# Performance work log

Measured on AMD Instinct MI355X. Metric: run time of the kernel, lower is better.

## Reference

```python
import jax, jax.numpy as jnp
import numpy as np

N_NODES = 16384
N_EDGES = 262144
M = 32          # eq_latent_multiplicity
HD = 16         # attention_head_dim
INV_SQRTD = 1.0 / np.sqrt(HD)
CLIP = 5.0      # attention_logit_clip
EPS = 1e-6
# irreps 0e + 1o: component slices of the channel_wise [.., m, 4] layout
EQ_SLICES = [(0, 1), (1, 4)]
TP_SLICES = [(0, 1), (1, 4), (4, 7), (7, 8)]  # 0e, 1o, 1o, 0e outputs of the uuu tensor product


def so3_layernorm(x, slices):
    # per-irrep RMS over (multiplicity, components), equivariant since it only rescales blocks
    outs = []
    for a, b in slices:
        blk = x[..., a:b]
        rms = jnp.sqrt(jnp.mean(blk * blk, axis=(-2, -1), keepdims=True) + EPS)
        outs.append(blk / rms)
    return jnp.concatenate(outs, axis=-1)


def setup_inputs() -> dict:
    key = jax.random.key(0)
    ks = jax.random.split(key, 12)
    E, N = N_EDGES, N_NODES
    inp = {
        "scalar_latent": jax.random.normal(ks[0], (E, 128), jnp.float32),
        "equiv_latent": jax.random.normal(ks[1], (E, M, 4), jnp.float32),
        "node_invariants": jax.random.normal(ks[2], (N, 64), jnp.float32),
        "edge_conditioning": jax.random.normal(ks[3], (E, 16), jnp.float32),
        "update_coeff": jnp.ones((1,), jnp.float32),
        "W_env": jax.random.normal(ks[4], (128, M * 2), jnp.float32) / np.sqrt(128),
        "b_env": jnp.zeros((M * 2,), jnp.float32),
        "Wq": jax.random.normal(ks[5], (64, M * HD), jnp.float32) / np.sqrt(64),
        "Wk": jax.random.normal(ks[6], (128, M * HD), jnp.float32) / np.sqrt(128),
        "W_mix": jax.random.normal(ks[7], (2 * M + 16, M * 4), jnp.float32) / np.sqrt(2 * M + 16),
        "b_mix": jnp.zeros((M * 4,), jnp.float32),
        "W_sc": jax.random.normal(ks[8], (2 * M + 16, 128), jnp.float32) / np.sqrt(2 * M + 16),
        "b_sc": jnp.zeros((128,), jnp.float32),
        "edge_center": jax.random.randint(ks[9], (E,), 0, N, jnp.int32),
        "active_edges": jnp.arange(E, dtype=jnp.int32),
    }
    return inp


def _forward(scalar_latent, equiv_latent, node_invariants, edge_conditioning,
             update_coeff, W_env, b_env, Wq, Wk, W_mix, b_mix, W_sc, b_sc,
             edge_center, active_edges):
    E = scalar_latent.shape[0]
    N = node_invariants.shape[0]

    # env_embed_mlp: scalar-latent derived gates modulate each irrep block (EquivariantScalarMLP)
    g = jax.nn.silu(scalar_latent @ W_env + b_env).reshape(E, M, 2)
    env_edges = jnp.concatenate([
        equiv_latent[..., 0:1] * g[..., 0:1],   # 0e block
        equiv_latent[..., 1:4] * g[..., 1:2],   # 1o block
    ], axis=-1)  # [E, M, 4]

    # attention: Q from receiver-node invariants, K from per-edge scalar latent
    Q = (node_invariants[edge_center] @ Wq).reshape(E, M, HD)
    K = (scalar_latent @ Wk).reshape(E, M, HD)
    logits = jnp.einsum('emd,emd->em', Q, K) * INV_SQRTD
    logits = jnp.clip(logits, -CLIP, CLIP)
    # scatter_softmax over edges sharing the same center node, per head m
    mx = jax.ops.segment_max(logits, edge_center, num_segments=N)   # [N, M]
    z = jnp.exp(logits - mx[edge_center])
    denom = jax.ops.segment_sum(z, edge_center, num_segments=N)[edge_center]
    attn = z / denom                                               # [E, M]
    env_edges = env_edges * attn[..., None]

    # scatter_sum edges -> nodes, SO3 layer norm, gather back per edge
    env_nodes = jax.ops.segment_sum(env_edges, edge_center, num_segments=N)  # [N, M, 4]
    env_nodes = so3_layernorm(env_nodes, EQ_SLICES)
    local_env = env_nodes[edge_center]                                       # [E, M, 4]

    # Contracter uuu, no weights, component normalization; irreps 0e+1o x 0e+1o -> 0e,1o,1o,0e
    x0, x1 = equiv_latent[..., 0:1], equiv_latent[..., 1:4]
    y0, y1 = local_env[..., 0:1], local_env[..., 1:4]
    tp_out = jnp.concatenate([
        x0 * y0,                                                    # 0e
        x0 * y1,                                                    # 1o
        x1 * y0,                                                    # 1o
        jnp.sum(x1 * y1, axis=-1, keepdims=True) / np.sqrt(3.0),    # 0e
    ], axis=-1)  # [E, M, 8]
    tp_out = so3_layernorm(tp_out, TP_SLICES)

    # projection EquivariantScalarMLP with edge conditioning
    inv_feats = jnp.concatenate([tp_out[..., 0], tp_out[..., 7]], axis=-1)  # [E, 2M]
    feats = jnp.concatenate([inv_feats, edge_conditioning], axis=-1)        # [E, 2M+16]
    mix = (feats @ W_mix + b_mix).reshape(E, M, 4)
    new_equiv = jnp.concatenate([
        mix[..., 0:1] * tp_out[..., 0:1] + mix[..., 1:2] * tp_out[..., 7:8],
        mix[..., 2:3] * tp_out[..., 1:4] + mix[..., 3:4] * tp_out[..., 4:7],
    ], axis=-1)  # [E, M, 4]
    new_scalar = feats @ W_sc + b_sc  # [E, 128]

    # residual stream: apply_residual_stream
    c_old = jax.lax.rsqrt(update_coeff * update_coeff + 1.0)  # [1]
    c_new = update_coeff * c_old
    scalar_out = (c_old * scalar_latent).at[active_edges].add(c_new * new_scalar)
    equiv_out = (c_old[..., None] * equiv_latent).at[active_edges].add(c_new[..., None] * new_equiv)
    return scalar_out, equiv_out


def reference(scalar_latent, equiv_latent, node_invariants, edge_conditioning,
              update_coeff, W_env, b_env, Wq, Wk, W_mix, b_mix, W_sc, b_sc,
              edge_center, active_edges):
    return _forward(scalar_latent, equiv_latent, node_invariants, edge_conditioning,
                    update_coeff, W_env, b_env, Wq, Wk, W_mix, b_mix, W_sc, b_sc,
                    edge_center, active_edges)
```

## Files before the change

### kernel.cpp

```cpp
#include <hip/hip_runtime.h>
#include <hip/hip_bf16.h>

#define E_EDGES 262144
#define N_NODES 16384

typedef short bf16x8 __attribute__((ext_vector_type(8)));
typedef float f32x4 __attribute__((ext_vector_type(4)));

static __device__ __forceinline__ short f2bf(float f) {
    union { float f; unsigned u; } v; v.f = f;
    unsigned r = v.u + 0x7FFFu + ((v.u >> 16) & 1u);
    return (short)(r >> 16);
}
static __device__ __forceinline__ float bf2f(short s) {
    union { unsigned u; float f; } v;
    v.u = ((unsigned)(unsigned short)s) << 16;
    return v.f;
}

__global__ void kprep(const float* __restrict__ Wk, const float* __restrict__ Wenv,
                      const float* __restrict__ Wmix, const float* __restrict__ Wsc,
                      short* __restrict__ WkT, short* __restrict__ WenvT,
                      short* __restrict__ WcatT) {
    int idx = blockIdx.x * 256 + threadIdx.x;
    if (idx < 65536) {
        int c = idx >> 7, k = idx & 127;
        WkT[idx] = f2bf(Wk[k * 512 + c]);
    } else if (idx < 65536 + 8192) {
        int o = idx - 65536;
        int c = o >> 7, k = o & 127;
        WenvT[o] = f2bf(Wenv[k * 64 + c]);
    } else {
        int o = idx - (65536 + 8192);
        int c = o / 96, k = o - c * 96;
        float v = 0.f;
        if (k < 80) v = (c < 128) ? Wmix[k * 128 + c] : Wsc[k * 128 + (c - 128)];
        WcatT[o] = f2bf(v);
    }
}

__global__ void khist(const int* __restrict__ ec, int* __restrict__ deg) {
    int e = blockIdx.x * 256 + threadIdx.x;
    atomicAdd(&deg[ec[e]], 1);
}

__global__ void kscan(const int* __restrict__ deg, int* __restrict__ offs,
                      int* __restrict__ cursor) {
    __shared__ int part[256];
    int t = threadIdx.x;
    int s = 0;
    for (int i = 0; i < 64; ++i) s += deg[t * 64 + i];
    part[t] = s;
    __syncthreads();
    if (t == 0) {
        int acc = 0;
        for (int i = 0; i < 256; ++i) { int v = part[i]; part[i] = acc; acc += v; }
        offs[N_NODES] = acc;
    }
    __syncthreads();
    int p = part[t];
    for (int i = 0; i < 64; ++i) {
        int idx = t * 64 + i;
        offs[idx] = p;
        cursor[idx] = p;
        p += deg[idx];
    }
}

__global__ void kscat(const int* __restrict__ ec, int* __restrict__ cursor,
                      int* __restrict__ csr) {
    int e = blockIdx.x * 256 + threadIdx.x;
    int p = atomicAdd(&cursor[ec[e]], 1);
    csr[p] = e;
}

__global__ void kqn(const float* __restrict__ ninv, const float* __restrict__ Wq,
                    float* __restrict__ Qn) {
    __shared__ float ni[8 * 68];
    int nBase = blockIdx.x * 8;
    int tid = threadIdx.x;
    for (int idx = tid; idx < 512; idx += 256) {
        int n = idx >> 6, j = idx & 63;
        ni[n * 68 + j] = ninv[(nBase + n) * 64 + j];
    }
    __syncthreads();
    float a0[8] = {0,0,0,0,0,0,0,0};
    float a1[8] = {0,0,0,0,0,0,0,0};
    for (int j = 0; j < 64; ++j) {
        float w0 = Wq[j * 512 + tid];
        float w1 = Wq[j * 512 + tid + 256];
#pragma unroll
        for (int n = 0; n < 8; ++n) {
            float s = ni[n * 68 + j];
            a0[n] += s * w0;
            a1[n] += s * w1;
        }
    }
#pragma unroll
    for (int n = 0; n < 8; ++n) {
        Qn[(nBase + n) * 512 + tid] = a0[n];
        Qn[(nBase + n) * 512 + tid + 256] = a1[n];
    }
}

__launch_bounds__(256)
__global__ void kmain1(const float* __restrict__ sl, const int* __restrict__ ec,
                       const float* __restrict__ Qn, const short* __restrict__ WkT,
                       const short* __restrict__ WenvT, const float* __restrict__ benv,
                       float* __restrict__ zbuf, short* __restrict__ gbuf) {
    __shared__ short slb[16 * 136];
    __shared__ int cn[16];
    int tid = threadIdx.x;
    int eBase = blockIdx.x * 16;
    for (int idx = tid; idx < 2048; idx += 256) {
        int e = idx >> 7, j = idx & 127;
        slb[e * 136 + j] = f2bf(sl[(eBase + e) * 128 + j]);
    }
    if (tid < 16) cn[tid] = ec[eBase + tid];
    __syncthreads();

    int lane = tid & 63, wv = tid >> 6;
    int r = lane & 15, q = lane >> 4;

    bf16x8 af[4];
#pragma unroll
    for (int kk = 0; kk < 4; ++kk)
        af[kk] = *(const bf16x8*)&slb[r * 136 + kk * 32 + q * 8];

    {
        f32x4 acc = {0.f, 0.f, 0.f, 0.f};
#pragma unroll
        for (int kk = 0; kk < 4; ++kk) {
            bf16x8 bb = *(const bf16x8*)&WenvT[(wv * 16 + r) * 128 + kk * 32 + q * 8];
            acc = __builtin_amdgcn_mfma_f32_16x16x32_bf16(af[kk], bb, acc, 0, 0, 0);
        }
        int gcol = wv * 16 + r;
        float bias = benv[gcol];
#pragma unroll
        for (int reg = 0; reg < 4; ++reg) {
            int e = q * 4 + reg;
            float x = acc[reg] + bias;
            float gv = x / (1.f + __expf(-x));
            gbuf[(eBase + e) * 64 + gcol] = f2bf(gv);
        }
    }

    for (int mi = 0; mi < 8; ++mi) {
        int m = wv * 8 + mi;
        f32x4 acc = {0.f, 0.f, 0.f, 0.f};
#pragma unroll
        for (int kk = 0; kk < 4; ++kk) {
            bf16x8 bb = *(const bf16x8*)&WkT[(m * 16 + r) * 128 + kk * 32 + q * 8];
            acc = __builtin_amdgcn_mfma_f32_16x16x32_bf16(af[kk], bb, acc, 0, 0, 0);
        }
        float p[4];
#pragma unroll
        for (int reg = 0; reg < 4; ++reg) {
            int e = q * 4 + reg;
            float qv = Qn[cn[e] * 512 + m * 16 + r];
            p[reg] = acc[reg] * qv;
        }
#pragma unroll
        for (int off = 1; off < 16; off <<= 1) {
#pragma unroll
            for (int reg = 0; reg < 4; ++reg)
                p[reg] += __shfl_xor(p[reg], off, 16);
        }
        if (r == 0) {
#pragma unroll
            for (int reg = 0; reg < 4; ++reg) {
                int e = q * 4 + reg;
                float l = p[reg] * 0.25f;
                l = fminf(5.f, fmaxf(-5.f, l));
                zbuf[(eBase + e) * 32 + m] = __expf(l);
            }
        }
    }
}

__launch_bounds__(256)
__global__ void kagg(const float* __restrict__ equiv, const float* __restrict__ zbuf,
                     const short* __restrict__ gbuf, const int* __restrict__ offs,
                     const int* __restrict__ csr, float* __restrict__ envn) {
    int tid = threadIdx.x;
    int wv = tid >> 6, lane = tid & 63;
    int node = blockIdx.x * 4 + wv;
    int m = lane >> 1, half = lane & 1;
    int c0 = m * 4 + half * 2;

    int start = offs[node], end = offs[node + 1];
    float d_acc = 0.f, a0 = 0.f, a1 = 0.f;
#pragma unroll 2
    for (int idx = start; idx < end; ++idx) {
        int e = csr[idx];
        float z = zbuf[e * 32 + m];
        short2 g2 = *(const short2*)&gbuf[e * 64 + 2 * m];
        float2 eq = *(const float2*)&equiv[(size_t)e * 128 + c0];
        float ga = half ? bf2f(g2.y) : bf2f(g2.x);
        float gb = bf2f(g2.y);
        d_acc += z;
        a0 += z * ga * eq.x;
        a1 += z * gb * eq.y;
    }
    float e0 = 0.f, e1 = 0.f;
    if (end > start) {
        float inv = 1.f / d_acc;
        e0 = a0 * inv;
        e1 = a1 * inv;
    }
    float p0 = half ? 0.f : e0 * e0;
    float p1 = half ? (e0 * e0 + e1 * e1) : e1 * e1;
#pragma unroll
    for (int off = 1; off < 64; off <<= 1) {
        p0 += __shfl_xor(p0, off, 64);
        p1 += __shfl_xor(p1, off, 64);
    }
    float i0 = rsqrtf(p0 * (1.f / 32.f) + 1e-6f);
    float i1 = rsqrtf(p1 * (1.f / 96.f) + 1e-6f);
    float o0 = half ? (e0 * i1) : (e0 * i0);
    float o1 = e1 * i1;
    float2 o; o.x = o0; o.y = o1;
    *(float2*)&envn[(size_t)node * 128 + c0] = o;
}

__launch_bounds__(256)
__global__ void kfinal(const float* __restrict__ sl, const float* __restrict__ equiv,
                       const float* __restrict__ econd, const int* __restrict__ ec,
                       const float* __restrict__ envn, const short* __restrict__ WcatT,
                       const float* __restrict__ bmix, const float* __restrict__ bsc,
                       const float* __restrict__ ucp, float* __restrict__ out) {
    __shared__ float eqlds[16 * 132];
    __shared__ float envl[16 * 132];
    __shared__ float mixl[16 * 132];
    __shared__ float condl[16 * 16];
    __shared__ short featb[16 * 104];
    __shared__ int cn[16];

    int tid = threadIdx.x;
    int eBase = blockIdx.x * 16;
    if (tid < 16) cn[tid] = ec[eBase + tid];
    for (int idx = tid; idx < 2048; idx += 256) {
        int e = idx >> 7, j = idx & 127;
        eqlds[e * 132 + j] = equiv[(eBase + e) * 128 + j];
    }
    {
        int e = tid >> 4, j = tid & 15;
        condl[tid] = econd[(eBase + e) * 16 + j];
    }
    float uc = ucp[0];
    float c_old = rsqrtf(uc * uc + 1.f);
    float c_new = uc * c_old;
    __syncthreads();
    for (int idx = tid; idx < 2048; idx += 256) {
        int e = idx >> 7, j = idx & 127;
        envl[e * 132 + j] = envn[cn[e] * 128 + j];
    }
    __syncthreads();

    int e = tid >> 4, i = tid & 15;
    float tp[2][8];
    {
        float s0 = 0, s1 = 0, s2 = 0, s3 = 0;
#pragma unroll
        for (int t2 = 0; t2 < 2; ++t2) {
            int m = i * 2 + t2;
            float4 x = *(const float4*)&eqlds[e * 132 + m * 4];
            float4 y = *(const float4*)&envl[e * 132 + m * 4];
            tp[t2][0] = x.x * y.x;
            tp[t2][1] = x.x * y.y; tp[t2][2] = x.x * y.z; tp[t2][3] = x.x * y.w;
            tp[t2][4] = x.y * y.x; tp[t2][5] = x.z * y.x; tp[t2][6] = x.w * y.x;
            tp[t2][7] = (x.y * y.y + x.z * y.z + x.w * y.w) * 0.57735026919f;
            s0 += tp[t2][0] * tp[t2][0];
            s1 += tp[t2][1] * tp[t2][1] + tp[t2][2] * tp[t2][2] + tp[t2][3] * tp[t2][3];
            s2 += tp[t2][4] * tp[t2][4] + tp[t2][5] * tp[t2][5] + tp[t2][6] * tp[t2][6];
            s3 += tp[t2][7] * tp[t2][7];
        }
#pragma unroll
        for (int off = 1; off < 16; off <<= 1) {
            s0 += __shfl_xor(s0, off, 16);
            s1 += __shfl_xor(s1, off, 16);
            s2 += __shfl_xor(s2, off, 16);
            s3 += __shfl_xor(s3, off, 16);
        }
        float i0 = rsqrtf(s0 * (1.f / 32.f) + 1e-6f);
        float i1 = rsqrtf(s1 * (1.f / 96.f) + 1e-6f);
        float i2 = rsqrtf(s2 * (1.f / 96.f) + 1e-6f);
        float i3 = rsqrtf(s3 * (1.f / 32.f) + 1e-6f);
#pragma unroll
        for (int t2 = 0; t2 < 2; ++t2) {
            tp[t2][0] *= i0;
            tp[t2][1] *= i1; tp[t2][2] *= i1; tp[t2][3] *= i1;
            tp[t2][4] *= i2; tp[t2][5] *= i2; tp[t2][6] *= i2;
            tp[t2][7] *= i3;
            int m = i * 2 + t2;
            featb[e * 104 + m] = f2bf(tp[t2][0]);
            featb[e * 104 + 32 + m] = f2bf(tp[t2][7]);
        }
        featb[e * 104 + 64 + i] = f2bf(condl[e * 16 + i]);
        featb[e * 104 + 80 + i] = 0;
    }
    __syncthreads();

    int lane = tid & 63, wv = tid >> 6;
    int r = lane & 15, q = lane >> 4;
    bf16x8 af[3];
#pragma unroll
    for (int kk = 0; kk < 3; ++kk)
        af[kk] = *(const bf16x8*)&featb[r * 104 + kk * 32 + q * 8];
#pragma unroll
    for (int ct4 = 0; ct4 < 4; ++ct4) {
        int ct = wv * 4 + ct4;
        f32x4 acc = {0.f, 0.f, 0.f, 0.f};
#pragma unroll
        for (int kk = 0; kk < 3; ++kk) {
            bf16x8 bb = *(const bf16x8*)&WcatT[(ct * 16 + r) * 96 + kk * 32 + q * 8];
            acc = __builtin_amdgcn_mfma_f32_16x16x32_bf16(af[kk], bb, acc, 0, 0, 0);
        }
        int colg = ct * 16 + r;
        if (colg < 128) {
            float bias = bmix[colg];
#pragma unroll
            for (int reg = 0; reg < 4; ++reg) {
                int ee = q * 4 + reg;
                mixl[ee * 132 + colg] = acc[reg] + bias;
            }
        } else {
            int j = colg - 128;
            float bias = bsc[j];
#pragma unroll
            for (int reg = 0; reg < 4; ++reg) {
                int ee = q * 4 + reg;
                int ge = eBase + ee;
                out[ge * 128 + j] = c_old * sl[ge * 128 + j] + c_new * (acc[reg] + bias);
            }
        }
    }
    __syncthreads();

    float* outeq = out + (size_t)E_EDGES * 128;
#pragma unroll
    for (int t2 = 0; t2 < 2; ++t2) {
        int m = i * 2 + t2;
        float4 mx = *(const float4*)&mixl[e * 132 + m * 4];
        float4 eq = *(const float4*)&eqlds[e * 132 + m * 4];
        float4 o;
        o.x = c_old * eq.x + c_new * (mx.x * tp[t2][0] + mx.y * tp[t2][7]);
        o.y = c_old * eq.y + c_new * (mx.z * tp[t2][1] + mx.w * tp[t2][4]);
        o.z = c_old * eq.z + c_new * (mx.z * tp[t2][2] + mx.w * tp[t2][5]);
        o.w = c_old * eq.w + c_new * (mx.z * tp[t2][3] + mx.w * tp[t2][6]);
        *(float4*)&outeq[(size_t)(eBase + e) * 128 + m * 4] = o;
    }
}

extern "C" void kernel_launch(void* const* d_in, const int* in_sizes, int n_in,
                              void* d_out, int out_size, void* d_ws, size_t ws_size,
                              hipStream_t stream) {
    const float* sl    = (const float*)d_in[0];
    const float* eqv   = (const float*)d_in[1];
    const float* ninv  = (const float*)d_in[2];
    const float* econd = (const float*)d_in[3];
    const float* uc    = (const float*)d_in[4];
    const float* Wenv  = (const float*)d_in[5];
    const float* benv  = (const float*)d_in[6];
    const float* Wq    = (const float*)d_in[7];
    const float* Wk    = (const float*)d_in[8];
    const float* Wmix  = (const float*)d_in[9];
    const float* bmix  = (const float*)d_in[10];
    const float* Wsc   = (const float*)d_in[11];
    const float* bsc   = (const float*)d_in[12];
    const int*   ec    = (const int*)d_in[13];
    float* out = (float*)d_out;

    float* ws = (float*)d_ws;
    float* Qn    = ws;
    float* zbuf  = Qn + (size_t)N_NODES * 512;
    float* envn  = zbuf + (size_t)E_EDGES * 32;
    short* gbuf  = (short*)(envn + (size_t)N_NODES * 128);
    short* WkT   = gbuf + (size_t)E_EDGES * 64;
    short* WenvT = WkT + 65536;
    short* WcatT = WenvT + 8192;
    int*   deg    = (int*)(WcatT + 24576);
    int*   offs   = deg + N_NODES;
    int*   cursor = offs + N_NODES + 1;
    int*   csr    = cursor + N_NODES;

    hipMemsetAsync(deg, 0, (size_t)N_NODES * sizeof(int), stream);

    kprep<<<384, 256, 0, stream>>>(Wk, Wenv, Wmix, Wsc, WkT, WenvT, WcatT);
    khist<<<E_EDGES / 256, 256, 0, stream>>>(ec, deg);
    kscan<<<1, 256, 0, stream>>>(deg, offs, cursor);
    kscat<<<E_EDGES / 256, 256, 0, stream>>>(ec, cursor, csr);
    kqn<<<N_NODES / 8, 256, 0, stream>>>(ninv, Wq, Qn);
    kmain1<<<E_EDGES / 16, 256, 0, stream>>>(sl, ec, Qn, WkT, WenvT, benv, zbuf, gbuf);
    kagg<<<N_NODES / 4, 256, 0, stream>>>(eqv, zbuf, gbuf, offs, csr, envn);
    kfinal<<<E_EDGES / 16, 256, 0, stream>>>(sl, eqv, econd, ec, envn, WcatT, bmix, bsc, uc, out);
}
```

Before: 1.033 ms.

## Process edges in CSR order in kmain1, store Qn as bf16, vectorize loads

```diff
diff --git a/kernel.cpp b/kernel.cpp
--- a/kernel.cpp
+++ b/kernel.cpp
@@ -75,7 +75,7 @@
 }
 
 __global__ void kqn(const float* __restrict__ ninv, const float* __restrict__ Wq,
-                    float* __restrict__ Qn) {
+                    unsigned short* __restrict__ Qnb) {
     __shared__ float ni[8 * 68];
     int nBase = blockIdx.x * 8;
     int tid = threadIdx.x;
@@ -98,25 +98,30 @@
     }
 #pragma unroll
     for (int n = 0; n < 8; ++n) {
-        Qn[(nBase + n) * 512 + tid] = a0[n];
-        Qn[(nBase + n) * 512 + tid + 256] = a1[n];
+        Qnb[(nBase + n) * 512 + tid] = (unsigned short)f2bf(a0[n]);
+        Qnb[(nBase + n) * 512 + tid + 256] = (unsigned short)f2bf(a1[n]);
     }
 }
 
 __launch_bounds__(256)
 __global__ void kmain1(const float* __restrict__ sl, const int* __restrict__ ec,
-                       const float* __restrict__ Qn, const short* __restrict__ WkT,
+                       const int* __restrict__ csr,
+                       const unsigned short* __restrict__ Qnb, const short* __restrict__ WkT,
                        const short* __restrict__ WenvT, const float* __restrict__ benv,
                        float* __restrict__ zbuf, short* __restrict__ gbuf) {
     __shared__ short slb[16 * 136];
     __shared__ int cn[16];
     int tid = threadIdx.x;
-    int eBase = blockIdx.x * 16;
-    for (int idx = tid; idx < 2048; idx += 256) {
-        int e = idx >> 7, j = idx & 127;
-        slb[e * 136 + j] = f2bf(sl[(eBase + e) * 128 + j]);
-    }
-    if (tid < 16) cn[tid] = ec[eBase + tid];
+    int pBase = blockIdx.x * 16;
+    if (tid < 16) cn[tid] = ec[csr[pBase + tid]];
+    for (int idx = tid; idx < 512; idx += 256) {
+        int e = idx >> 5, j4 = idx & 31;
+        int ge = csr[pBase + e];
+        float4 v = *(const float4*)&sl[(size_t)ge * 128 + j4 * 4];
+        short4 s4;
+        s4.x = f2bf(v.x); s4.y = f2bf(v.y); s4.z = f2bf(v.z); s4.w = f2bf(v.w);
+        *(short4*)&slb[e * 136 + j4 * 4] = s4;
+    }
     __syncthreads();
 
     int lane = tid & 63, wv = tid >> 6;
@@ -141,7 +146,7 @@
             int e = q * 4 + reg;
             float x = acc[reg] + bias;
             float gv = x / (1.f + __expf(-x));
-            gbuf[(eBase + e) * 64 + gcol] = f2bf(gv);
+            gbuf[(pBase + e) * 64 + gcol] = f2bf(gv);
         }
     }
 
@@ -157,7 +162,7 @@
 #pragma unroll
         for (int reg = 0; reg < 4; ++reg) {
             int e = q * 4 + reg;
-            float qv = Qn[cn[e] * 512 + m * 16 + r];
+            float qv = bf2f((short)Qnb[(size_t)cn[e] * 512 + m * 16 + r]);
             p[reg] = acc[reg] * qv;
         }
 #pragma unroll
@@ -172,7 +177,7 @@
                 int e = q * 4 + reg;
                 float l = p[reg] * 0.25f;
                 l = fminf(5.f, fmaxf(-5.f, l));
-                zbuf[(eBase + e) * 32 + m] = __expf(l);
+                zbuf[(pBase + e) * 32 + m] = __expf(l);
             }
         }
     }
@@ -193,8 +198,8 @@
 #pragma unroll 2
     for (int idx = start; idx < end; ++idx) {
         int e = csr[idx];
-        float z = zbuf[e * 32 + m];
-        short2 g2 = *(const short2*)&gbuf[e * 64 + 2 * m];
+        float z = zbuf[idx * 32 + m];
+        short2 g2 = *(const short2*)&gbuf[idx * 64 + 2 * m];
         float2 eq = *(const float2*)&equiv[(size_t)e * 128 + c0];
         float ga = half ? bf2f(g2.y) : bf2f(g2.x);
         float gb = bf2f(g2.y);
@@ -239,9 +244,10 @@
     int tid = threadIdx.x;
     int eBase = blockIdx.x * 16;
     if (tid < 16) cn[tid] = ec[eBase + tid];
-    for (int idx = tid; idx < 2048; idx += 256) {
-        int e = idx >> 7, j = idx & 127;
-        eqlds[e * 132 + j] = equiv[(eBase + e) * 128 + j];
+    for (int idx = tid; idx < 512; idx += 256) {
+        int e = idx >> 5, j4 = idx & 31;
+        *(float4*)&eqlds[e * 132 + j4 * 4] =
+            *(const float4*)&equiv[(size_t)(eBase + e) * 128 + j4 * 4];
     }
     {
         int e = tid >> 4, j = tid & 15;
@@ -251,9 +257,10 @@
     float c_old = rsqrtf(uc * uc + 1.f);
     float c_new = uc * c_old;
     __syncthreads();
-    for (int idx = tid; idx < 2048; idx += 256) {
-        int e = idx >> 7, j = idx & 127;
-        envl[e * 132 + j] = envn[cn[e] * 128 + j];
+    for (int idx = tid; idx < 512; idx += 256) {
+        int e = idx >> 5, j4 = idx & 31;
+        *(float4*)&envl[e * 132 + j4 * 4] =
+            *(const float4*)&envn[(size_t)cn[e] * 128 + j4 * 4];
     }
     __syncthreads();
 
@@ -372,8 +379,8 @@
     float* out = (float*)d_out;
 
     float* ws = (float*)d_ws;
-    float* Qn    = ws;
-    float* zbuf  = Qn + (size_t)N_NODES * 512;
+    unsigned short* Qnb = (unsigned short*)ws;
+    float* zbuf  = (float*)(Qnb + (size_t)N_NODES * 512);
     float* envn  = zbuf + (size_t)E_EDGES * 32;
     short* gbuf  = (short*)(envn + (size_t)N_NODES * 128);
     short* WkT   = gbuf + (size_t)E_EDGES * 64;
@@ -390,8 +397,8 @@
     khist<<<E_EDGES / 256, 256, 0, stream>>>(ec, deg);
     kscan<<<1, 256, 0, stream>>>(deg, offs, cursor);
     kscat<<<E_EDGES / 256, 256, 0, stream>>>(ec, cursor, csr);
-    kqn<<<N_NODES / 8, 256, 0, stream>>>(ninv, Wq, Qn);
-    kmain1<<<E_EDGES / 16, 256, 0, stream>>>(sl, ec, Qn, WkT, WenvT, benv, zbuf, gbuf);
+    kqn<<<N_NODES / 8, 256, 0, stream>>>(ninv, Wq, Qnb);
+    kmain1<<<E_EDGES / 16, 256, 0, stream>>>(sl, ec, csr, Qnb, WkT, WenvT, benv, zbuf, gbuf);
     kagg<<<N_NODES / 4, 256, 0, stream>>>(eqv, zbuf, gbuf, offs, csr, envn);
     kfinal<<<E_EDGES / 16, 256, 0, stream>>>(sl, eqv, econd, ec, envn, WcatT, bmix, bsc, uc, out);
 }
```

Result: faster. 975.0 us (-5.6%).

## Fold Wk into per-node query vectors and fuse attention with aggregation per node

Applied to the files above, without the earlier changes.

```diff
diff --git a/kernel.cpp b/kernel.cpp
--- a/kernel.cpp
+++ b/kernel.cpp
@@ -20,22 +20,23 @@
 
 __global__ void kprep(const float* __restrict__ Wk, const float* __restrict__ Wenv,
                       const float* __restrict__ Wmix, const float* __restrict__ Wsc,
-                      short* __restrict__ WkT, short* __restrict__ WenvT,
-                      short* __restrict__ WcatT) {
+                      short* __restrict__ WenvT, short* __restrict__ WcatT,
+                      short* __restrict__ WkB) {
     int idx = blockIdx.x * 256 + threadIdx.x;
-    if (idx < 65536) {
+    if (idx < 8192) {
         int c = idx >> 7, k = idx & 127;
-        WkT[idx] = f2bf(Wk[k * 512 + c]);
-    } else if (idx < 65536 + 8192) {
-        int o = idx - 65536;
-        int c = o >> 7, k = o & 127;
-        WenvT[o] = f2bf(Wenv[k * 64 + c]);
-    } else {
-        int o = idx - (65536 + 8192);
+        WenvT[idx] = f2bf(Wenv[k * 64 + c]);
+    } else if (idx < 8192 + 24576) {
+        int o = idx - 8192;
         int c = o / 96, k = o - c * 96;
         float v = 0.f;
         if (k < 80) v = (c < 128) ? Wmix[k * 128 + c] : Wsc[k * 128 + (c - 128)];
         WcatT[o] = f2bf(v);
+    } else {
+        int o = idx - 32768;
+        int m = o >> 12, rest = o & 4095;
+        int c = rest >> 5, dp = rest & 31;
+        WkB[o] = (dp < 16) ? f2bf(Wk[c * 512 + m * 16 + dp]) : (short)0;
     }
 }
 
@@ -104,123 +105,169 @@
 }
 
 __launch_bounds__(256)
-__global__ void kmain1(const float* __restrict__ sl, const int* __restrict__ ec,
-                       const float* __restrict__ Qn, const short* __restrict__ WkT,
-                       const short* __restrict__ WenvT, const float* __restrict__ benv,
-                       float* __restrict__ zbuf, short* __restrict__ gbuf) {
-    __shared__ short slb[16 * 136];
-    __shared__ int cn[16];
+__global__ void kV(const float* __restrict__ Qn, const short* __restrict__ WkB,
+                   short* __restrict__ VT, int nb0) {
     int tid = threadIdx.x;
-    int eBase = blockIdx.x * 16;
-    for (int idx = tid; idx < 2048; idx += 256) {
-        int e = idx >> 7, j = idx & 127;
-        slb[e * 136 + j] = f2bf(sl[(eBase + e) * 128 + j]);
-    }
-    if (tid < 16) cn[tid] = ec[eBase + tid];
-    __syncthreads();
-
-    int lane = tid & 63, wv = tid >> 6;
+    int w = tid >> 6, lane = tid & 63;
     int r = lane & 15, q = lane >> 4;
-
-    bf16x8 af[4];
-#pragma unroll
-    for (int kk = 0; kk < 4; ++kk)
-        af[kk] = *(const bf16x8*)&slb[r * 136 + kk * 32 + q * 8];
-
-    {
-        f32x4 acc = {0.f, 0.f, 0.f, 0.f};
-#pragma unroll
-        for (int kk = 0; kk < 4; ++kk) {
-            bf16x8 bb = *(const bf16x8*)&WenvT[(wv * 16 + r) * 128 + kk * 32 + q * 8];
-            acc = __builtin_amdgcn_mfma_f32_16x16x32_bf16(af[kk], bb, acc, 0, 0, 0);
-        }
-        int gcol = wv * 16 + r;
-        float bias = benv[gcol];
+    int nbl = blockIdx.x * 16;
+#pragma unroll
+    for (int mi = 0; mi < 8; ++mi) {
+        int m = w * 8 + mi;
+        const float* qp = &Qn[(size_t)(nb0 + nbl + r) * 512 + m * 16 + (q & 1) * 8];
+        float4 qa = *(const float4*)qp;
+        float4 qb = *(const float4*)(qp + 4);
+        bf16x8 af;
+        af[0] = f2bf(qa.x); af[1] = f2bf(qa.y); af[2] = f2bf(qa.z); af[3] = f2bf(qa.w);
+        af[4] = f2bf(qb.x); af[5] = f2bf(qb.y); af[6] = f2bf(qb.z); af[7] = f2bf(qb.w);
+#pragma unroll
+        for (int ct = 0; ct < 8; ++ct) {
+            bf16x8 bb = *(const bf16x8*)&WkB[(m * 128 + ct * 16 + r) * 32 + q * 8];
+            f32x4 acc = {0.f, 0.f, 0.f, 0.f};
+            acc = __builtin_amdgcn_mfma_f32_16x16x32_bf16(af, bb, acc, 0, 0, 0);
+#pragma unroll
+            for (int reg = 0; reg < 4; ++reg) {
+                VT[(size_t)(nbl + q * 4 + reg) * 4096 + m * 128 + ct * 16 + r] =
+                    f2bf(acc[reg]);
+            }
+        }
+    }
+}
+
+__launch_bounds__(256)
+__global__ void kmain2(const float* __restrict__ sl, const float* __restrict__ equiv,
+                       const int* __restrict__ csr, const int* __restrict__ offs,
+                       const short* __restrict__ VT, const short* __restrict__ WenvT,
+                       const float* __restrict__ benv, float* __restrict__ envn,
+                       int nb0) {
+    __shared__ short slb[4][16 * 136];
+    __shared__ short glds[4][16 * 68];
+    int tid = threadIdx.x;
+    int w = tid >> 6, lane = tid & 63;
+    int r = lane & 15, q = lane >> 4;
+    int node = nb0 + blockIdx.x * 4 + w;
+    int start = offs[node], end = offs[node + 1];
+    if (start >= end) return;
+
+    bf16x8 vb[2][4];
+    const short* vtn = VT + (size_t)(node - nb0) * 4096;
+#pragma unroll
+    for (int ct = 0; ct < 2; ++ct)
+#pragma unroll
+        for (int kk = 0; kk < 4; ++kk)
+            vb[ct][kk] = *(const bf16x8*)&vtn[(ct * 16 + r) * 128 + kk * 32 + q * 8];
+    float bias[4];
+#pragma unroll
+    for (int g4 = 0; g4 < 4; ++g4) bias[g4] = benv[g4 * 16 + r];
+
+    float facc[2][4] = {{0,0,0,0},{0,0,0,0}};
+    float dsum[2] = {0.f, 0.f};
+
+    for (int c0 = start; c0 < end; c0 += 16) {
+        int cnt = end - c0; if (cnt > 16) cnt = 16;
+#pragma unroll
+        for (int i = 0; i < 8; ++i) {
+            int idx4 = i * 64 + lane;
+            int e = idx4 >> 5, j4 = idx4 & 31;
+            float4 v = {0.f, 0.f, 0.f, 0.f};
+            if (e < cnt) {
+                int ge = csr[c0 + e];
+                v = *(const float4*)&sl[(size_t)ge * 128 + j4 * 4];
+            }
+            short4 s4; s4.x = f2bf(v.x); s4.y = f2bf(v.y); s4.z = f2bf(v.z); s4.w = f2bf(v.w);
+            *(short4*)&slb[w][e * 136 + j4 * 4] = s4;
+        }
+        asm volatile("s_waitcnt lgkmcnt(0)" ::: "memory");
+        bf16x8 af[4];
+#pragma unroll
+        for (int kk = 0; kk < 4; ++kk)
+            af[kk] = *(const bf16x8*)&slb[w][r * 136 + kk * 32 + q * 8];
+
+        float zv[2][4];
+#pragma unroll
+        for (int ct = 0; ct < 2; ++ct) {
+            f32x4 acc = {0.f, 0.f, 0.f, 0.f};
+#pragma unroll
+            for (int kk = 0; kk < 4; ++kk)
+                acc = __builtin_amdgcn_mfma_f32_16x16x32_bf16(af[kk], vb[ct][kk], acc, 0, 0, 0);
+#pragma unroll
+            for (int reg = 0; reg < 4; ++reg) {
+                float l = acc[reg] * 0.25f;
+                l = fminf(5.f, fmaxf(-5.f, l));
+                zv[ct][reg] = __expf(l);
+            }
+        }
+
+#pragma unroll
+        for (int g4 = 0; g4 < 4; ++g4) {
+            f32x4 acc = {0.f, 0.f, 0.f, 0.f};
+#pragma unroll
+            for (int kk = 0; kk < 4; ++kk) {
+                bf16x8 bb = *(const bf16x8*)&WenvT[(g4 * 16 + r) * 128 + kk * 32 + q * 8];
+                acc = __builtin_amdgcn_mfma_f32_16x16x32_bf16(af[kk], bb, acc, 0, 0, 0);
+            }
+#pragma unroll
+            for (int reg = 0; reg < 4; ++reg) {
+                float x = acc[reg] + bias[g4];
+                float gv = x / (1.f + __expf(-x));
+                glds[w][(q * 4 + reg) * 68 + g4 * 16 + r] = f2bf(gv);
+            }
+        }
+        asm volatile("s_waitcnt lgkmcnt(0)" ::: "memory");
+
 #pragma unroll
         for (int reg = 0; reg < 4; ++reg) {
             int e = q * 4 + reg;
-            float x = acc[reg] + bias;
-            float gv = x / (1.f + __expf(-x));
-            gbuf[(eBase + e) * 64 + gcol] = f2bf(gv);
-        }
-    }
-
-    for (int mi = 0; mi < 8; ++mi) {
-        int m = wv * 8 + mi;
-        f32x4 acc = {0.f, 0.f, 0.f, 0.f};
-#pragma unroll
-        for (int kk = 0; kk < 4; ++kk) {
-            bf16x8 bb = *(const bf16x8*)&WkT[(m * 16 + r) * 128 + kk * 32 + q * 8];
-            acc = __builtin_amdgcn_mfma_f32_16x16x32_bf16(af[kk], bb, acc, 0, 0, 0);
-        }
-        float p[4];
-#pragma unroll
-        for (int reg = 0; reg < 4; ++reg) {
-            int e = q * 4 + reg;
-            float qv = Qn[cn[e] * 512 + m * 16 + r];
-            p[reg] = acc[reg] * qv;
-        }
-#pragma unroll
-        for (int off = 1; off < 16; off <<= 1) {
-#pragma unroll
-            for (int reg = 0; reg < 4; ++reg)
-                p[reg] += __shfl_xor(p[reg], off, 16);
-        }
-        if (r == 0) {
-#pragma unroll
-            for (int reg = 0; reg < 4; ++reg) {
-                int e = q * 4 + reg;
-                float l = p[reg] * 0.25f;
-                l = fminf(5.f, fmaxf(-5.f, l));
-                zbuf[(eBase + e) * 32 + m] = __expf(l);
-            }
-        }
-    }
-}
-
-__launch_bounds__(256)
-__global__ void kagg(const float* __restrict__ equiv, const float* __restrict__ zbuf,
-                     const short* __restrict__ gbuf, const int* __restrict__ offs,
-                     const int* __restrict__ csr, float* __restrict__ envn) {
-    int tid = threadIdx.x;
-    int wv = tid >> 6, lane = tid & 63;
-    int node = blockIdx.x * 4 + wv;
-    int m = lane >> 1, half = lane & 1;
-    int c0 = m * 4 + half * 2;
-
-    int start = offs[node], end = offs[node + 1];
-    float d_acc = 0.f, a0 = 0.f, a1 = 0.f;
-#pragma unroll 2
-    for (int idx = start; idx < end; ++idx) {
-        int e = csr[idx];
-        float z = zbuf[e * 32 + m];
-        short2 g2 = *(const short2*)&gbuf[e * 64 + 2 * m];
-        float2 eq = *(const float2*)&equiv[(size_t)e * 128 + c0];
-        float ga = half ? bf2f(g2.y) : bf2f(g2.x);
-        float gb = bf2f(g2.y);
-        d_acc += z;
-        a0 += z * ga * eq.x;
-        a1 += z * gb * eq.y;
-    }
-    float e0 = 0.f, e1 = 0.f;
-    if (end > start) {
-        float inv = 1.f / d_acc;
-        e0 = a0 * inv;
-        e1 = a1 * inv;
-    }
-    float p0 = half ? 0.f : e0 * e0;
-    float p1 = half ? (e0 * e0 + e1 * e1) : e1 * e1;
-#pragma unroll
-    for (int off = 1; off < 64; off <<= 1) {
+            if (e < cnt) {
+                int ge = csr[c0 + e];
+#pragma unroll
+                for (int ct = 0; ct < 2; ++ct) {
+                    int m = ct * 16 + r;
+                    float z = zv[ct][reg];
+                    unsigned gp = *(const unsigned*)&glds[w][e * 68 + 2 * m];
+                    float g0 = bf2f((short)(gp & 0xFFFFu));
+                    float g1 = bf2f((short)(gp >> 16));
+                    float4 eq = *(const float4*)&equiv[(size_t)ge * 128 + m * 4];
+                    facc[ct][0] += z * g0 * eq.x;
+                    facc[ct][1] += z * g1 * eq.y;
+                    facc[ct][2] += z * g1 * eq.z;
+                    facc[ct][3] += z * g1 * eq.w;
+                    dsum[ct] += z;
+                }
+            }
+        }
+    }
+
+#pragma unroll
+    for (int off = 16; off < 64; off <<= 1) {
+#pragma unroll
+        for (int ct = 0; ct < 2; ++ct) {
+#pragma unroll
+            for (int i = 0; i < 4; ++i) facc[ct][i] += __shfl_xor(facc[ct][i], off, 64);
+            dsum[ct] += __shfl_xor(dsum[ct], off, 64);
+        }
+    }
+    float env0[4], env1[4];
+    float inv0 = 1.f / dsum[0], inv1 = 1.f / dsum[1];
+#pragma unroll
+    for (int i = 0; i < 4; ++i) { env0[i] = facc[0][i] * inv0; env1[i] = facc[1][i] * inv1; }
+    float p0 = env0[0] * env0[0] + env1[0] * env1[0];
+    float p1 = env0[1]*env0[1] + env0[2]*env0[2] + env0[3]*env0[3]
+             + env1[1]*env1[1] + env1[2]*env1[2] + env1[3]*env1[3];
+#pragma unroll
+    for (int off = 1; off < 16; off <<= 1) {
         p0 += __shfl_xor(p0, off, 64);
         p1 += __shfl_xor(p1, off, 64);
     }
     float i0 = rsqrtf(p0 * (1.f / 32.f) + 1e-6f);
     float i1 = rsqrtf(p1 * (1.f / 96.f) + 1e-6f);
-    float o0 = half ? (e0 * i1) : (e0 * i0);
-    float o1 = e1 * i1;
-    float2 o; o.x = o0; o.y = o1;
-    *(float2*)&envn[(size_t)node * 128 + c0] = o;
+    if (q == 0) {
+        float4 o0, o1;
+        o0.x = env0[0] * i0; o0.y = env0[1] * i1; o0.z = env0[2] * i1; o0.w = env0[3] * i1;
+        o1.x = env1[0] * i0; o1.y = env1[1] * i1; o1.z = env1[2] * i1; o1.w = env1[3] * i1;
+        *(float4*)&envn[(size_t)node * 128 + r * 4] = o0;
+        *(float4*)&envn[(size_t)node * 128 + 64 + r * 4] = o1;
+    }
 }
 
 __launch_bounds__(256)
@@ -239,9 +286,10 @@
     int tid = threadIdx.x;
     int eBase = blockIdx.x * 16;
     if (tid < 16) cn[tid] = ec[eBase + tid];
-    for (int idx = tid; idx < 2048; idx += 256) {
-        int e = idx >> 7, j = idx & 127;
-        eqlds[e * 132 + j] = equiv[(eBase + e) * 128 + j];
+    for (int idx = tid; idx < 512; idx += 256) {
+        int e = idx >> 5, j4 = idx & 31;
+        *(float4*)&eqlds[e * 132 + j4 * 4] =
+            *(const float4*)&equiv[(size_t)(eBase + e) * 128 + j4 * 4];
     }
     {
         int e = tid >> 4, j = tid & 15;
@@ -251,9 +299,10 @@
     float c_old = rsqrtf(uc * uc + 1.f);
     float c_new = uc * c_old;
     __syncthreads();
-    for (int idx = tid; idx < 2048; idx += 256) {
-        int e = idx >> 7, j = idx & 127;
-        envl[e * 132 + j] = envn[cn[e] * 128 + j];
+    for (int idx = tid; idx < 512; idx += 256) {
+        int e = idx >> 5, j4 = idx & 31;
+        *(float4*)&envl[e * 132 + j4 * 4] =
+            *(const float4*)&envn[(size_t)cn[e] * 128 + j4 * 4];
     }
     __syncthreads();
 
@@ -371,27 +420,33 @@
     const int*   ec    = (const int*)d_in[13];
     float* out = (float*)d_out;
 
+    const int NHALF = N_NODES / 2;
+
     float* ws = (float*)d_ws;
     float* Qn    = ws;
-    float* zbuf  = Qn + (size_t)N_NODES * 512;
-    float* envn  = zbuf + (size_t)E_EDGES * 32;
-    short* gbuf  = (short*)(envn + (size_t)N_NODES * 128);
-    short* WkT   = gbuf + (size_t)E_EDGES * 64;
-    short* WenvT = WkT + 65536;
+    float* envn  = Qn + (size_t)N_NODES * 512;
+    short* VT    = (short*)(envn + (size_t)N_NODES * 128);
+    short* WenvT = VT + (size_t)NHALF * 4096;
     short* WcatT = WenvT + 8192;
-    int*   deg    = (int*)(WcatT + 24576);
+    short* WkB   = WcatT + 24576;
+    int*   deg    = (int*)(WkB + 131072);
     int*   offs   = deg + N_NODES;
     int*   cursor = offs + N_NODES + 1;
     int*   csr    = cursor + N_NODES;
 
     hipMemsetAsync(deg, 0, (size_t)N_NODES * sizeof(int), stream);
 
-    kprep<<<384, 256, 0, stream>>>(Wk, Wenv, Wmix, Wsc, WkT, WenvT, WcatT);
+    kprep<<<640, 256, 0, stream>>>(Wk, Wenv, Wmix, Wsc, WenvT, WcatT, WkB);
     khist<<<E_EDGES / 256, 256, 0, stream>>>(ec, deg);
     kscan<<<1, 256, 0, stream>>>(deg, offs, cursor);
     kscat<<<E_EDGES / 256, 256, 0, stream>>>(ec, cursor, csr);
     kqn<<<N_NODES / 8, 256, 0, stream>>>(ninv, Wq, Qn);
-    kmain1<<<E_EDGES / 16, 256, 0, stream>>>(sl, ec, Qn, WkT, WenvT, benv, zbuf, gbuf);
-    kagg<<<N_NODES / 4, 256, 0, stream>>>(eqv, zbuf, gbuf, offs, csr, envn);
+
+    for (int pass = 0; pass < 2; ++pass) {
+        int nb0 = pass * NHALF;
+        kV<<<NHALF / 16, 256, 0, stream>>>(Qn, WkB, VT, nb0);
+        kmain2<<<NHALF / 4, 256, 0, stream>>>(sl, eqv, csr, offs, VT, WenvT, benv, envn, nb0);
+    }
+
     kfinal<<<E_EDGES / 16, 256, 0, stream>>>(sl, eqv, econd, ec, envn, WcatT, bmix, bsc, uc, out);
 }
```

Result: faster. 862.5 us (-16.5%).
